# Kernel optimization log

Hardware: AMD Instinct MI355X
Metric: run time of the kernel (lower is better)

The kernel has to match this reference:

```python
import jax, jax.numpy as jnp
import numpy as np
import math

B, S, D, H = 2, 2048, 1024, 16
DK = D // H
EPS = 1e-5

def setup_inputs() -> dict:
    key = jax.random.key(0)
    ks = jax.random.split(key, 16)
    s = 0.02
    return {
        'query': jax.random.normal(ks[0], (B, S, D), jnp.float32),
        'key': jax.random.normal(ks[1], (B, S, D), jnp.float32),
        'value': jax.random.normal(ks[2], (B, S, D), jnp.float32),
        'mask': jax.random.randint(ks[3], (B, 1, S, S), 0, 2, jnp.int32),
        'market_context': jax.random.normal(ks[4], (B, D), jnp.float32),
        'Wq': jax.random.normal(ks[5], (D, D), jnp.float32) * s,
        'bq': jnp.zeros((D,), jnp.float32),
        'Wk': jax.random.normal(ks[6], (D, D), jnp.float32) * s,
        'bk': jnp.zeros((D,), jnp.float32),
        'Wv': jax.random.normal(ks[7], (D, D), jnp.float32) * s,
        'bv': jnp.zeros((D,), jnp.float32),
        'Wo': jax.random.normal(ks[8], (D, D), jnp.float32) * s,
        'bo': jnp.zeros((D,), jnp.float32),
        'Wc': jax.random.normal(ks[9], (D, D), jnp.float32) * s,
        'bc': jnp.zeros((D,), jnp.float32),
        'ln_g': jnp.ones((D,), jnp.float32),
        'ln_b': jnp.zeros((D,), jnp.float32),
    }

def reference(query, key, value, mask, market_context,
              Wq, bq, Wk, bk, Wv, bv, Wo, bo, Wc, bc, ln_g, ln_b):
    b, s, d = query.shape
    # QKV projections -> [B, H, S, DK]
    Q = (query @ Wq + bq).reshape(b, s, H, DK).transpose(0, 2, 1, 3)
    K = (key @ Wk + bk).reshape(b, s, H, DK).transpose(0, 2, 1, 3)
    V = (value @ Wv + bv).reshape(b, s, H, DK).transpose(0, 2, 1, 3)
    # market context -> per-head bias added to K (broadcast over sequence)
    ctx = (market_context @ Wc + bc).reshape(b, H, DK)
    K = K + ctx[:, :, None, :]
    scores = jnp.einsum('bhqd,bhkd->bhqk', Q, K) / math.sqrt(DK)
    scores = jnp.where(mask == 0, jnp.float32(-1e9), scores)
    attn = jax.nn.softmax(scores, axis=-1)  # dropout is identity in eval
    ctx2 = jnp.einsum('bhqk,bhkd->bhqd', attn, V)
    ctx2 = ctx2.transpose(0, 2, 1, 3).reshape(b, s, d)
    out = ctx2 @ Wo + bo
    x = out + query
    mu = jnp.mean(x, axis=-1, keepdims=True)
    var = jnp.mean((x - mu) ** 2, axis=-1, keepdims=True)
    return (x - mu) * jax.lax.rsqrt(var + EPS) * ln_g + ln_b
```

## Files before the change

kernel.cpp:

```cpp
#include <hip/hip_runtime.h>
#include <cstdint>

typedef unsigned short u16;
typedef __attribute__((ext_vector_type(8))) short s16x8;
typedef __attribute__((ext_vector_type(8))) unsigned short u16x8;
typedef __attribute__((ext_vector_type(4))) float f32x4;
typedef __attribute__((ext_vector_type(16))) float f32x16;
typedef __attribute__((ext_vector_type(2))) unsigned uint2v;
typedef __attribute__((ext_vector_type(4))) unsigned uint4v;

__device__ inline u16 f2bf(float f){
  union { float f; uint32_t u; } v; v.f = f;
  uint32_t r = v.u + 0x7fffu + ((v.u >> 16) & 1u);
  return (u16)(r >> 16);
}

__device__ inline f32x4 mfma16(s16x8 a, s16x8 b, f32x4 c){
  return __builtin_amdgcn_mfma_f32_16x16x32_bf16(a, b, c, 0, 0, 0);
}
__device__ inline f32x16 mfma32(s16x8 a, s16x8 b, f32x16 c){
  return __builtin_amdgcn_mfma_f32_32x32x16_bf16(a, b, c, 0, 0, 0);
}
__device__ inline unsigned cvtpk(float a, float b){
  unsigned r;
  asm("v_cvt_pk_bf16_f32 %0, %1, %2" : "=v"(r) : "v"(a), "v"(b));
  return r;
}
__device__ inline float exp2a(float x){
  float r;
  asm("v_exp_f32 %0, %1" : "=v"(r) : "v"(x));
  return r;
}
__device__ inline void glds16(const u16* g, u16* l){
  __builtin_amdgcn_global_load_lds((const __attribute__((address_space(1))) void*)g,
                                   (__attribute__((address_space(3))) void*)l, 16, 0, 0);
}
__device__ inline void glds4(const unsigned* g, unsigned* l){
  __builtin_amdgcn_global_load_lds((const __attribute__((address_space(1))) void*)g,
                                   (__attribute__((address_space(3))) void*)l, 4, 0, 0);
}

__global__ __launch_bounds__(256) void convert3_kernel(
    const float* __restrict__ q, const float* __restrict__ k, const float* __restrict__ v,
    u16* __restrict__ qo, u16* __restrict__ ko, u16* __restrict__ vo){
  const float* src = (blockIdx.y == 0) ? q : (blockIdx.y == 1) ? k : v;
  u16* dst = (blockIdx.y == 0) ? qo : (blockIdx.y == 1) ? ko : vo;
  size_t i = ((size_t)blockIdx.x * 256 + threadIdx.x) * 8;
  float4 a = *(const float4*)(src + i);
  float4 b = *(const float4*)(src + i + 4);
  u16x8 o = { f2bf(a.x), f2bf(a.y), f2bf(a.z), f2bf(a.w),
              f2bf(b.x), f2bf(b.y), f2bf(b.z), f2bf(b.w) };
  *(u16x8*)(dst + i) = o;
}

__global__ void transw_kernel(
    const float* __restrict__ W0, const float* __restrict__ W1,
    const float* __restrict__ W2, const float* __restrict__ W3,
    u16* __restrict__ T0, u16* __restrict__ T1, u16* __restrict__ T2, u16* __restrict__ T3){
  const float* W = (blockIdx.z == 0) ? W0 : (blockIdx.z == 1) ? W1 : (blockIdx.z == 2) ? W2 : W3;
  u16* T = (blockIdx.z == 0) ? T0 : (blockIdx.z == 1) ? T1 : (blockIdx.z == 2) ? T2 : T3;
  __shared__ float t[32][33];
  int n0 = blockIdx.x * 32, k0 = blockIdx.y * 32;
  int tx = threadIdx.x, ty = threadIdx.y;
  #pragma unroll
  for (int j = 0; j < 4; j++)
    t[ty + j*8][tx] = W[(size_t)(k0 + ty + j*8) * 1024 + n0 + tx];
  __syncthreads();
  #pragma unroll
  for (int j = 0; j < 4; j++)
    T[(size_t)(n0 + ty + j*8) * 1024 + k0 + tx] = f2bf(t[tx][ty + j*8]);
}

__global__ __launch_bounds__(256) void packmask_kernel(const int* __restrict__ mask,
                                                       unsigned* __restrict__ bits){
  size_t i = (size_t)blockIdx.x * 256 + threadIdx.x;
  int v = mask[i];
  unsigned long long bal = __ballot(v != 0);
  int lane = threadIdx.x & 63;
  if (lane == 0)       bits[i >> 5] = (unsigned)bal;
  else if (lane == 32) bits[i >> 5] = (unsigned)(bal >> 32);
}

__global__ __launch_bounds__(256) void ctx_kernel(const float* __restrict__ mc,
                                                  const float* __restrict__ Wc,
                                                  const float* __restrict__ bc,
                                                  float* __restrict__ ctx){
  int c = threadIdx.x & 63, kk = threadIdx.x >> 6;
  int col = blockIdx.x * 64 + c;
  float a0 = 0.f, a1 = 0.f;
  for (int k = kk * 256; k < kk * 256 + 256; k++){
    float wv = Wc[(size_t)k * 1024 + col];
    a0 += mc[k] * wv;
    a1 += mc[1024 + k] * wv;
  }
  __shared__ float red[2][4][64];
  red[0][kk][c] = a0; red[1][kk][c] = a1;
  __syncthreads();
  if (threadIdx.x < 64){
    int cc = threadIdx.x;
    ctx[blockIdx.x*64 + cc] = red[0][0][cc] + red[0][1][cc] + red[0][2][cc] + red[0][3][cc]
                              + bc[blockIdx.x*64 + cc];
  } else if (threadIdx.x < 128){
    int cc = threadIdx.x - 64;
    ctx[1024 + blockIdx.x*64 + cc] = red[1][0][cc] + red[1][1][cc] + red[1][2][cc] + red[1][3][cc]
                                     + bc[blockIdx.x*64 + cc];
  }
}

struct GemmParams {
  const u16* A0; const u16* A1; const u16* A2; const u16* A3;
  const u16* W0; const u16* W1; const u16* W2; const u16* W3;
  const float* b0; const float* b1; const float* b2;
  const float* ctx;
  u16* outQ; u16* outK; u16* outV; float* outX0; float* outX1;
  int which;
};

__global__ __launch_bounds__(256) void gemm_kernel(GemmParams P){
  int o = blockIdx.x + (blockIdx.y << 3) + (blockIdx.z << 8);
  int xcd = o & 7, j = o >> 3;
  int by = xcd + ((j & 3) << 3);
  int bx = (j >> 2) & 7;
  int bz = j >> 5;

  int z, kbase, nkt;
  const u16* A; const u16* W;
  if (P.which < 0){
    z = bz; kbase = 0; nkt = 16;
    if (z == 0){ A = P.A0; W = P.W0; }
    else if (z == 1){ A = P.A1; W = P.W1; }
    else { A = P.A2; W = P.W2; }
  } else {
    z = 3; kbase = bz * 512; nkt = 8;
    A = P.A3; W = P.W3;
  }
  int m0 = by * 128, n0 = bx * 128;
  __shared__ __align__(16) u16 sm[16384];
  u16* Asm = sm;
  u16* Bsm = sm + 8192;
  int tid = threadIdx.x, lane = tid & 63, w = tid >> 6;
  int li = lane & 15, lq = lane >> 4;
  int wm = w >> 1, wn = w & 1;
  f32x4 zero = {0.f, 0.f, 0.f, 0.f};
  f32x4 acc[4][4];
  #pragma unroll
  for (int i = 0; i < 4; i++)
    #pragma unroll
    for (int jj = 0; jj < 4; jj++) acc[i][jj] = zero;

  for (int kt = 0; kt < nkt; ++kt){
    int k0 = kbase + kt * 64;
    __syncthreads();
    #pragma unroll
    for (int i = 0; i < 4; i++){
      int u0 = i * 256 + (w << 6);
      int u = u0 + lane, row = u >> 3, slot = u & 7;
      glds16(A + (size_t)(m0 + row) * 1024 + k0 + ((slot ^ (row & 7)) << 3), &Asm[u0 * 8]);
      glds16(W + (size_t)(n0 + row) * 1024 + k0 + ((slot ^ (row & 7)) << 3), &Bsm[u0 * 8]);
    }
    __syncthreads();
    #pragma unroll
    for (int ks = 0; ks < 2; ++ks){
      s16x8 af[4], bfr[4];
      #pragma unroll
      for (int mb = 0; mb < 4; mb++){
        int row = wm * 64 + mb * 16 + li, slot = ks * 4 + lq;
        af[mb] = *(const s16x8*)&Asm[row * 64 + ((slot ^ (row & 7)) << 3)];
      }
      #pragma unroll
      for (int nb = 0; nb < 4; nb++){
        int row = wn * 64 + nb * 16 + li, slot = ks * 4 + lq;
        bfr[nb] = *(const s16x8*)&Bsm[row * 64 + ((slot ^ (row & 7)) << 3)];
      }
      #pragma unroll
      for (int mb = 0; mb < 4; mb++)
        #pragma unroll
        for (int nb = 0; nb < 4; nb++)
          acc[mb][nb] = mfma16(af[mb], bfr[nb], acc[mb][nb]);
    }
  }

  if (z == 2){
    const float* bias = P.b2;
    __syncthreads();
    u16* Ot = sm;
    #pragma unroll
    for (int mb = 0; mb < 4; mb++){
      #pragma unroll
      for (int nb = 0; nb < 4; nb++){
        int colL = wn * 64 + nb * 16 + li;
        int rowB = wm * 64 + mb * 16 + lq * 4;
        float bcol = bias[n0 + colL];
        unsigned p01 = cvtpk(acc[mb][nb][0] + bcol, acc[mb][nb][1] + bcol);
        unsigned p23 = cvtpk(acc[mb][nb][2] + bcol, acc[mb][nb][3] + bcol);
        int ba = colL * 256 + ((rowB * 2) ^ ((colL & 7) << 4));
        *(unsigned*)((char*)Ot + ba) = p01;
        *(unsigned*)((char*)Ot + ba + 4) = p23;
      }
    }
    __syncthreads();
    int bq_ = m0 >> 11, srow0 = m0 & 2047;
    #pragma unroll
    for (int i = 0; i < 8; i++){
      int u = i * 256 + tid;
      int colL = u >> 4, sc = u & 15;
      int ba = colL * 256 + ((sc * 16) ^ ((colL & 7) << 4));
      u16x8 vv = *(const u16x8*)((char*)Ot + ba);
      *(u16x8*)(P.outV + (((size_t)(bq_ * 1024 + n0 + colL)) << 11) + srow0 + sc * 8) = vv;
    }
    return;
  }

  if (z == 3){
    float* Xo = (kbase == 0) ? P.outX0 : P.outX1;
    #pragma unroll
    for (int mb = 0; mb < 4; mb++){
      #pragma unroll
      for (int nb = 0; nb < 4; nb++){
        int col = n0 + wn * 64 + nb * 16 + li;
        #pragma unroll
        for (int r = 0; r < 4; r++){
          int row = m0 + wm * 64 + mb * 16 + lq * 4 + r;
          Xo[(size_t)row * 1024 + col] = acc[mb][nb][r];
        }
      }
    }
    return;
  }

  const float* bias = (z == 0) ? P.b0 : P.b1;
  #pragma unroll
  for (int mb = 0; mb < 4; mb++){
    #pragma unroll
    for (int nb = 0; nb < 4; nb++){
      int colL = wn * 64 + nb * 16 + li; int col = n0 + colL;
      float bcol = bias[col];
      #pragma unroll
      for (int r = 0; r < 4; r++){
        int row = m0 + wm * 64 + mb * 16 + lq * 4 + r;
        float v = acc[mb][nb][r] + bcol;
        if (z == 0){
          P.outQ[(size_t)row * 1024 + col] = f2bf(v);
        } else {
          v += P.ctx[(size_t)(row >> 11) * 1024 + col];
          P.outK[(size_t)row * 1024 + col] = f2bf(v);
        }
      }
    }
  }
}

__global__ __launch_bounds__(256) void attn_kernel(
    const u16* __restrict__ Qg, const u16* __restrict__ Kg, const u16* __restrict__ Vtg,
    const unsigned* __restrict__ mbits, u16* __restrict__ ctx2){
  __shared__ __align__(16) u16 arena[17408];
  int tid = threadIdx.x, lane = tid & 63, w = tid >> 6;
  int l31 = lane & 31, hi = lane >> 5;
  int r7 = l31 & 7;
  int orig = blockIdx.x + (blockIdx.y << 4);
  int swz = (orig & 7) * 64 + (orig >> 3);
  int q0 = (swz & 15) * 128, bh = swz >> 4, b = bh >> 4, h = bh & 15;
  const float CK = 0.18033688011f;
  const float MK = 64.f * CK;

  s16x8 qf[4];
  {
    const u16* qp = Qg + (size_t)(b * 2048 + q0 + w * 32 + l31) * 1024 + h * 64 + hi * 8;
    #pragma unroll
    for (int ks = 0; ks < 4; ks++)
      qf[ks] = *(const s16x8*)(qp + ks * 16);
  }

  auto STAGE = [&](int kt, int buf){
    int kv0 = kt * 64;
    u16* Kbuf = &arena[buf * 8192];
    u16* Vbuf = &arena[buf * 8192 + 4096];
    unsigned* Ms = (unsigned*)&arena[16384] + buf * 256;
    #pragma unroll
    for (int i = 0; i < 2; i++){
      int u0 = (w * 2 + i) * 64;
      int u = u0 + lane, row = u >> 3, slot = u & 7;
      int scol = (slot ^ (row & 7)) << 3;
      glds16(Kg + (size_t)(b * 2048 + kv0 + row) * 1024 + h * 64 + scol, &Kbuf[u0 * 8]);
      glds16(Vtg + (((size_t)(bh * 64 + row)) << 11) + kv0 + scol, &Vbuf[u0 * 8]);
    }
    {
      int u = w * 64 + lane;
      glds4(mbits + (size_t)(b * 2048 + q0 + (u >> 1)) * 64 + kt * 2 + (u & 1), Ms + w * 64);
    }
  };

  f32x16 accO[2];
  #pragma unroll
  for (int d = 0; d < 2; d++)
    #pragma unroll
    for (int r = 0; r < 16; r++) accO[d][r] = 0.f;
  float lsum = 0.f;

  STAGE(0, 0);

  for (int t = 0; t < 32; ++t){
    int cur = t & 1;
    __builtin_amdgcn_s_barrier();
    if (t < 31){
      STAGE(t + 1, cur ^ 1);
      asm volatile("s_waitcnt vmcnt(5)" ::: "memory");
    } else {
      asm volatile("s_waitcnt vmcnt(0)" ::: "memory");
    }
    __builtin_amdgcn_sched_barrier(0);
    __builtin_amdgcn_s_barrier();
    const u16* Kbuf = &arena[cur * 8192];
    const u16* Vbuf = &arena[cur * 8192 + 4096];
    const unsigned* Ms = (const unsigned*)&arena[16384] + cur * 256;
    int qr = w * 32 + l31;

    f32x16 S[2];
    __builtin_amdgcn_s_setprio(1);
    #pragma unroll
    for (int j = 0; j < 2; j++){
      #pragma unroll
      for (int r = 0; r < 16; r++) S[j][r] = 0.f;
      #pragma unroll
      for (int ks = 0; ks < 4; ks++){
        s16x8 kf = *(const s16x8*)&Kbuf[(j * 32 + l31) * 64 + (((ks * 2 + hi) ^ r7) << 3)];
        S[j] = mfma32(kf, qf[ks], S[j]);
      }
    }
    __builtin_amdgcn_s_setprio(0);

    uint2v mw = *(const uint2v*)(Ms + qr * 2);
    unsigned mh0 = mw[0] >> (hi << 2), mh1 = mw[1] >> (hi << 2);
    float ts[4] = {0.f, 0.f, 0.f, 0.f};
    #pragma unroll
    for (int j = 0; j < 2; j++){
      unsigned mh = j ? mh1 : mh0;
      #pragma unroll
      for (int rg = 0; rg < 16; rg++){
        int pos = (rg & 3) + ((rg >> 2) << 3);
        float pv = exp2a(S[j][rg] * CK - MK);
        pv = ((mh >> pos) & 1u) ? pv : 0.f;
        S[j][rg] = pv;
        ts[rg & 3] += pv;
      }
    }
    float tsum = (ts[0] + ts[1]) + (ts[2] + ts[3]);
    tsum += __shfl_xor(tsum, 32, 64);
    lsum += tsum;

    s16x8 pf[4];
    #pragma unroll
    for (int j = 0; j < 2; j++){
      #pragma unroll
      for (int hs = 0; hs < 2; hs++){
        int rb = hs * 8;
        unsigned A0 = cvtpk(S[j][rb + 0], S[j][rb + 1]);
        unsigned A1 = cvtpk(S[j][rb + 2], S[j][rb + 3]);
        unsigned B0 = cvtpk(S[j][rb + 4], S[j][rb + 5]);
        unsigned B1 = cvtpk(S[j][rb + 6], S[j][rb + 7]);
        uint2v r01 = __builtin_amdgcn_permlane32_swap(A0, B0, false, false);
        uint2v r23 = __builtin_amdgcn_permlane32_swap(A1, B1, false, false);
        uint4v uu = { r01[0], r23[0], r01[1], r23[1] };
        pf[j * 2 + hs] = *(s16x8*)&uu;
      }
    }
    __builtin_amdgcn_s_setprio(1);
    #pragma unroll
    for (int c = 0; c < 4; c++){
      #pragma unroll
      for (int dh = 0; dh < 2; dh++){
        s16x8 vf = *(const s16x8*)&Vbuf[(dh * 32 + l31) * 64 + (((c * 2 + hi) ^ r7) << 3)];
        accO[dh] = mfma32(vf, pf[c], accO[dh]);
      }
    }
    __builtin_amdgcn_s_setprio(0);
  }

  __syncthreads();
  float inv = 1.f / lsum;
  u16* Ot = arena;
  int qr = w * 32 + l31;
  #pragma unroll
  for (int dh = 0; dh < 2; dh++){
    #pragma unroll
    for (int rg = 0; rg < 16; rg += 2){
      int dk = dh * 32 + (rg & 3) + ((rg >> 2) << 3) + (hi << 2);
      unsigned pk = cvtpk(accO[dh][rg] * inv, accO[dh][rg + 1] * inv);
      *(unsigned*)&Ot[qr * 64 + (((dk >> 3) ^ (qr & 7)) << 3) + (dk & 7)] = pk;
    }
  }
  __syncthreads();
  #pragma unroll
  for (int i = 0; i < 4; i++){
    int u = i * 256 + tid, row = u >> 3, slot = u & 7;
    u16x8 vv = *(const u16x8*)&Ot[row * 64 + ((slot ^ (row & 7)) << 3)];
    *(u16x8*)(ctx2 + (size_t)(b * 2048 + q0 + row) * 1024 + h * 64 + slot * 8) = vv;
  }
}

__global__ __launch_bounds__(256) void ln_kernel(const float* __restrict__ X0,
                                                 const float* __restrict__ X1,
                                                 const float* __restrict__ qres,
                                                 const float* __restrict__ bo,
                                                 const float* __restrict__ g,
                                                 const float* __restrict__ bb,
                                                 float* __restrict__ out){
  size_t row = blockIdx.x;
  int tid = threadIdx.x;
  float4 a = *(const float4*)(X0 + row * 1024 + tid * 4);
  float4 c = *(const float4*)(X1 + row * 1024 + tid * 4);
  float4 q = *(const float4*)(qres + row * 1024 + tid * 4);
  float4 bv = *(const float4*)(bo + tid * 4);
  float4 v;
  v.x = a.x + c.x + q.x + bv.x;
  v.y = a.y + c.y + q.y + bv.y;
  v.z = a.z + c.z + q.z + bv.z;
  v.w = a.w + c.w + q.w + bv.w;
  float s = v.x + v.y + v.z + v.w;
  float s2 = v.x*v.x + v.y*v.y + v.z*v.z + v.w*v.w;
  #pragma unroll
  for (int o = 1; o < 64; o <<= 1){
    s += __shfl_xor(s, o, 64);
    s2 += __shfl_xor(s2, o, 64);
  }
  __shared__ float rs[4], rs2[4];
  int w = tid >> 6;
  if ((tid & 63) == 0){ rs[w] = s; rs2[w] = s2; }
  __syncthreads();
  s = rs[0] + rs[1] + rs[2] + rs[3];
  s2 = rs2[0] + rs2[1] + rs2[2] + rs2[3];
  float mu = s * (1.f / 1024.f);
  float var = s2 * (1.f / 1024.f) - mu * mu;
  float rstd = rsqrtf(var + 1e-5f);
  float4 gg = *(const float4*)(g + tid * 4);
  float4 bt = *(const float4*)(bb + tid * 4);
  float4 o;
  o.x = (v.x - mu) * rstd * gg.x + bt.x;
  o.y = (v.y - mu) * rstd * gg.y + bt.y;
  o.z = (v.z - mu) * rstd * gg.z + bt.z;
  o.w = (v.w - mu) * rstd * gg.w + bt.w;
  *(float4*)(out + row * 1024 + tid * 4) = o;
}

extern "C" void kernel_launch(void* const* d_in, const int* in_sizes, int n_in,
                              void* d_out, int out_size, void* d_ws, size_t ws_size,
                              hipStream_t stream){
  const float* query = (const float*)d_in[0];
  const float* key_  = (const float*)d_in[1];
  const float* value = (const float*)d_in[2];
  const int*   mask  = (const int*)d_in[3];
  const float* mc    = (const float*)d_in[4];
  const float* Wq = (const float*)d_in[5];  const float* bq = (const float*)d_in[6];
  const float* Wk = (const float*)d_in[7];  const float* bk = (const float*)d_in[8];
  const float* Wv = (const float*)d_in[9];  const float* bv = (const float*)d_in[10];
  const float* Wo = (const float*)d_in[11]; const float* bo = (const float*)d_in[12];
  const float* Wc = (const float*)d_in[13]; const float* bc = (const float*)d_in[14];
  const float* lng = (const float*)d_in[15]; const float* lnb = (const float*)d_in[16];
  float* outp = (float*)d_out;
  uint8_t* ws = (uint8_t*)d_ws;
  const size_t MB = (size_t)1 << 20;
  if (ws_size < 58 * MB) return;

  u16* q_bf = (u16*)(ws + 0);
  u16* k_bf = (u16*)(ws + 8 * MB);
  u16* v_bf = (u16*)(ws + 16 * MB);
  float* X0 = (float*)(ws + 8 * MB);
  u16* Qb   = (u16*)(ws + 24 * MB);
  u16* Kb   = (u16*)(ws + 32 * MB);
  float* X1 = (float*)(ws + 32 * MB);
  u16* Vt   = (u16*)(ws + 40 * MB);
  u16* Wqt  = (u16*)(ws + 48 * MB);
  u16* Wkt  = (u16*)(ws + 50 * MB);
  u16* Wvt  = (u16*)(ws + 52 * MB);
  u16* Wot  = (u16*)(ws + 54 * MB);
  unsigned* mbits = (unsigned*)(ws + 56 * MB);
  float* ctxf = (float*)(ws + 57 * MB);
  u16* ctx2 = q_bf;

  convert3_kernel<<<dim3(2048, 3), 256, 0, stream>>>(query, key_, value, q_bf, k_bf, v_bf);
  transw_kernel<<<dim3(32, 32, 4), dim3(32, 8), 0, stream>>>(Wq, Wk, Wv, Wo, Wqt, Wkt, Wvt, Wot);
  packmask_kernel<<<32768, 256, 0, stream>>>(mask, mbits);
  ctx_kernel<<<16, 256, 0, stream>>>(mc, Wc, bc, ctxf);

  GemmParams gp;
  gp.A0 = q_bf; gp.A1 = k_bf; gp.A2 = v_bf; gp.A3 = ctx2;
  gp.W0 = Wqt;  gp.W1 = Wkt;  gp.W2 = Wvt;  gp.W3 = Wot;
  gp.b0 = bq;   gp.b1 = bk;   gp.b2 = bv;
  gp.ctx = ctxf;
  gp.outQ = Qb; gp.outK = Kb; gp.outV = Vt; gp.outX0 = X0; gp.outX1 = X1;
  gp.which = -1;
  gemm_kernel<<<dim3(8, 32, 3), 256, 0, stream>>>(gp);

  attn_kernel<<<dim3(16, 32), 256, 0, stream>>>(Qb, Kb, Vt, mbits, ctx2);

  gp.which = 3;
  gemm_kernel<<<dim3(8, 32, 2), 256, 0, stream>>>(gp);

  ln_kernel<<<4096, 256, 0, stream>>>(X0, X1, query, bo, lng, lnb, outp);
}
```

Measured before the change: 180.6 us.

## Double-buffer GEMM K-tiles and compute softmax row sums via MFMA with ones

The projection GEMM moves from a single 64-wide K tile with two block syncs per step to double-buffered 32-wide K tiles. The next tile's global-to-LDS load overlaps the current tile's MFMAs, with a new XOR swizzle for the narrower rows. In the attention kernel, the scalar per-lane row-sum reduction and cross-lane shuffle are replaced by an extra MFMA against a ones vector. That moves softmax denominator work onto the matrix unit and sums the same bf16-rounded probabilities used for P·V. The cost is twice as many loop iterations and barriers in the GEMM, plus one extra MFMA per chunk in attention.

```diff
diff --git a/kernel.cpp b/kernel.cpp
--- a/kernel.cpp
+++ b/kernel.cpp
@@ -126,18 +126,16 @@
   int z, kbase, nkt;
   const u16* A; const u16* W;
   if (P.which < 0){
-    z = bz; kbase = 0; nkt = 16;
+    z = bz; kbase = 0; nkt = 32;
     if (z == 0){ A = P.A0; W = P.W0; }
     else if (z == 1){ A = P.A1; W = P.W1; }
     else { A = P.A2; W = P.W2; }
   } else {
-    z = 3; kbase = bz * 512; nkt = 8;
+    z = 3; kbase = bz * 512; nkt = 16;
     A = P.A3; W = P.W3;
   }
   int m0 = by * 128, n0 = bx * 128;
   __shared__ __align__(16) u16 sm[16384];
-  u16* Asm = sm;
-  u16* Bsm = sm + 8192;
   int tid = threadIdx.x, lane = tid & 63, w = tid >> 6;
   int li = lane & 15, lq = lane >> 4;
   int wm = w >> 1, wn = w & 1;
@@ -148,36 +146,53 @@
     #pragma unroll
     for (int jj = 0; jj < 4; jj++) acc[i][jj] = zero;
 
+  auto STAGE = [&](int kt, int buf){
+    int k0 = kbase + kt * 32;
+    u16* Ab = &sm[buf * 8192];
+    u16* Bb = &sm[buf * 8192 + 4096];
+    #pragma unroll
+    for (int i = 0; i < 2; i++){
+      int u0 = i * 256 + (w << 6);
+      int u = u0 + lane, row = u >> 2, slot = u & 3;
+      int scol = (slot ^ ((row >> 1) & 3)) << 3;
+      glds16(A + (size_t)(m0 + row) * 1024 + k0 + scol, &Ab[u0 * 8]);
+      glds16(W + (size_t)(n0 + row) * 1024 + k0 + scol, &Bb[u0 * 8]);
+    }
+  };
+
+  STAGE(0, 0);
+
   for (int kt = 0; kt < nkt; ++kt){
-    int k0 = kbase + kt * 64;
-    __syncthreads();
-    #pragma unroll
-    for (int i = 0; i < 4; i++){
-      int u0 = i * 256 + (w << 6);
-      int u = u0 + lane, row = u >> 3, slot = u & 7;
-      glds16(A + (size_t)(m0 + row) * 1024 + k0 + ((slot ^ (row & 7)) << 3), &Asm[u0 * 8]);
-      glds16(W + (size_t)(n0 + row) * 1024 + k0 + ((slot ^ (row & 7)) << 3), &Bsm[u0 * 8]);
-    }
-    __syncthreads();
-    #pragma unroll
-    for (int ks = 0; ks < 2; ++ks){
-      s16x8 af[4], bfr[4];
-      #pragma unroll
-      for (int mb = 0; mb < 4; mb++){
-        int row = wm * 64 + mb * 16 + li, slot = ks * 4 + lq;
-        af[mb] = *(const s16x8*)&Asm[row * 64 + ((slot ^ (row & 7)) << 3)];
-      }
-      #pragma unroll
-      for (int nb = 0; nb < 4; nb++){
-        int row = wn * 64 + nb * 16 + li, slot = ks * 4 + lq;
-        bfr[nb] = *(const s16x8*)&Bsm[row * 64 + ((slot ^ (row & 7)) << 3)];
-      }
-      #pragma unroll
-      for (int mb = 0; mb < 4; mb++)
-        #pragma unroll
-        for (int nb = 0; nb < 4; nb++)
-          acc[mb][nb] = mfma16(af[mb], bfr[nb], acc[mb][nb]);
-    }
+    int cur = kt & 1;
+    __builtin_amdgcn_s_barrier();
+    if (kt + 1 < nkt){
+      STAGE(kt + 1, cur ^ 1);
+      asm volatile("s_waitcnt vmcnt(4)" ::: "memory");
+    } else {
+      asm volatile("s_waitcnt vmcnt(0)" ::: "memory");
+    }
+    __builtin_amdgcn_sched_barrier(0);
+    __builtin_amdgcn_s_barrier();
+    const u16* Ab = &sm[cur * 8192];
+    const u16* Bb = &sm[cur * 8192 + 4096];
+    s16x8 af[4], bfr[4];
+    #pragma unroll
+    for (int mb = 0; mb < 4; mb++){
+      int row = wm * 64 + mb * 16 + li;
+      af[mb] = *(const s16x8*)&Ab[row * 32 + ((lq ^ ((row >> 1) & 3)) << 3)];
+    }
+    #pragma unroll
+    for (int nb = 0; nb < 4; nb++){
+      int row = wn * 64 + nb * 16 + li;
+      bfr[nb] = *(const s16x8*)&Bb[row * 32 + ((lq ^ ((row >> 1) & 3)) << 3)];
+    }
+    __builtin_amdgcn_s_setprio(1);
+    #pragma unroll
+    for (int mb = 0; mb < 4; mb++)
+      #pragma unroll
+      for (int nb = 0; nb < 4; nb++)
+        acc[mb][nb] = mfma16(af[mb], bfr[nb], acc[mb][nb]);
+    __builtin_amdgcn_s_setprio(0);
   }
 
   if (z == 2){
@@ -270,6 +285,9 @@
     for (int ks = 0; ks < 4; ks++)
       qf[ks] = *(const s16x8*)(qp + ks * 16);
   }
+  s16x8 onesf;
+  #pragma unroll
+  for (int e = 0; e < 8; e++) onesf[e] = (short)0x3F80;
 
   auto STAGE = [&](int kt, int buf){
     int kv0 = kt * 64;
@@ -290,12 +308,13 @@
     }
   };
 
-  f32x16 accO[2];
+  f32x16 accO[2], accS;
   #pragma unroll
   for (int d = 0; d < 2; d++)
     #pragma unroll
     for (int r = 0; r < 16; r++) accO[d][r] = 0.f;
-  float lsum = 0.f;
+  #pragma unroll
+  for (int r = 0; r < 16; r++) accS[r] = 0.f;
 
   STAGE(0, 0);
 
@@ -331,7 +350,6 @@
 
     uint2v mw = *(const uint2v*)(Ms + qr * 2);
     unsigned mh0 = mw[0] >> (hi << 2), mh1 = mw[1] >> (hi << 2);
-    float ts[4] = {0.f, 0.f, 0.f, 0.f};
     #pragma unroll
     for (int j = 0; j < 2; j++){
       unsigned mh = j ? mh1 : mh0;
@@ -339,14 +357,9 @@
       for (int rg = 0; rg < 16; rg++){
         int pos = (rg & 3) + ((rg >> 2) << 3);
         float pv = exp2a(S[j][rg] * CK - MK);
-        pv = ((mh >> pos) & 1u) ? pv : 0.f;
-        S[j][rg] = pv;
-        ts[rg & 3] += pv;
-      }
-    }
-    float tsum = (ts[0] + ts[1]) + (ts[2] + ts[3]);
-    tsum += __shfl_xor(tsum, 32, 64);
-    lsum += tsum;
+        S[j][rg] = ((mh >> pos) & 1u) ? pv : 0.f;
+      }
+    }
 
     s16x8 pf[4];
     #pragma unroll
@@ -372,11 +385,13 @@
         s16x8 vf = *(const s16x8*)&Vbuf[(dh * 32 + l31) * 64 + (((c * 2 + hi) ^ r7) << 3)];
         accO[dh] = mfma32(vf, pf[c], accO[dh]);
       }
+      accS = mfma32(onesf, pf[c], accS);
     }
     __builtin_amdgcn_s_setprio(0);
   }
 
   __syncthreads();
+  float lsum = accS[0];
   float inv = 1.f / lsum;
   u16* Ot = arena;
   int qr = w * 32 + l31;
```

Measured after the change: 181.0 us. Within noise of the previous version (+0.2%).
